# Kernel optimization log

Hardware: AMD Instinct MI355X
Metric: run time of the kernel (lower is better)

## Reference

```python
import jax, jax.numpy as jnp
from jax import lax
import numpy as np

KS = 15          # dark-channel window
PAD = (KS - 1) // 2
TEMP = 10000.0   # positional encoding temperature
NPF = 32         # max(num_pos_feats_x, y, z)
EPS = 1e-6


def _conv1x1(x, w, b):
    # x: [B,C,H,W], w: [O,C], b: [O]
    return jnp.einsum('bchw,oc->bohw', x, w) + b[None, :, None, None]


def _conv2s2(x, w, b):
    # kernel 2, stride 2, no padding; w: [O,I,2,2]
    y = lax.conv_general_dilated(x, w, (2, 2), 'VALID',
                                 dimension_numbers=('NCHW', 'OIHW', 'NCHW'))
    return y + b[None, :, None, None]


def _lrelu(x):
    return jnp.where(x >= 0, x, 0.1 * x)


def _resize(x, h, w):
    return jax.image.resize(x, (x.shape[0], x.shape[1], h, w), method='bilinear')


def _dark_channel(x):
    # min over channels, reflect pad, 15x15 sliding min (== unfold+min in torch)
    dm = jnp.min(x, axis=1, keepdims=True)  # [B,1,H,W]
    dm = jnp.pad(dm, ((0, 0), (0, 0), (PAD, PAD), (PAD, PAD)), mode='reflect')
    return lax.reduce_window(dm, jnp.inf, lax.min,
                             (1, 1, KS, KS), (1, 1, 1, 1), 'VALID')


def _sincos(e, d, dim_t):
    # e: [B,H,W] -> [B,H,W,d] with interleaved sin/cos (torch stack+flatten)
    p = e[..., None] / dim_t[:d]
    return jnp.stack((jnp.sin(p[..., 0::2]), jnp.cos(p[..., 1::2])),
                     axis=4).reshape(e.shape + (d,))


def _pos_encoding(x, dark):
    B, _, H, W = x.shape
    scale = 2.0 * np.pi
    yv = jnp.arange(H, dtype=jnp.float32)
    xv = jnp.arange(W, dtype=jnp.float32)
    ye = jnp.broadcast_to((yv / (yv[-1] + EPS) * scale)[None, :, None], (B, H, W))
    xe = jnp.broadcast_to((xv / (xv[-1] + EPS) * scale)[None, None, :], (B, H, W))
    z = dark[:, 0]
    ze = z / (jnp.max(z, axis=(1, 2), keepdims=True) + EPS) * scale
    dim_t = TEMP ** (2.0 * (jnp.arange(NPF, dtype=jnp.float32) // 2) / NPF)
    pos_x = _sincos(xe, 16, dim_t)
    pos_y = _sincos(ye, 16, dim_t)
    pos_z = _sincos(ze, 32, dim_t)
    return jnp.concatenate((pos_x, pos_y, pos_z), axis=3).transpose(0, 3, 1, 2)


def _forward(x, w_cf1, b_cf1, w_e1, b_e1, w_e2, b_e2, w_d1, b_d1, w_d2, b_d2,
             w_pha1, b_pha1, w_pha2, b_pha2, w_amp1, b_amp1, w_amp2, b_amp2,
             w_spat1, b_spat1, w_spat2, b_spat2, w_u1, b_u1, w_u2, b_u2,
             w_u3, b_u3, w_u4, b_u4, w_cf2, b_cf2, w_cf3, b_cf3):
    xori = x
    dark = _dark_channel(1.0 - x)            # DCP of inverted image [B,1,512,512]
    ape = _pos_encoding(x, dark) + _conv1x1(x, w_cf1, b_cf1)  # [B,64,H,W]

    x_f = _conv1x1(_conv1x1(x, w_e1, b_e1), w_e2, b_e2)       # [B,64,512,512]
    x_d1 = _conv2s2(x_f, w_d1, b_d1)                          # [B,128,256,256]
    x_d2 = _conv2s2(x_d1, w_d2, b_d2)                         # [B,256,128,128]
    Hd, Wd = x_d2.shape[2], x_d2.shape[3]

    x_freq = jnp.fft.rfft2(x_d2)             # norm='backward' (default)
    x_pha = jnp.angle(x_freq)
    x_amp = jnp.abs(x_freq)
    # phase branch is computed but unused downstream (matches original code)
    x_pha = _conv1x1(_lrelu(_conv1x1(x_pha, w_pha1, b_pha1)), w_pha2, b_pha2)
    x_amp = _conv1x1(_lrelu(_conv1x1(x_amp, w_amp1, b_amp1)), w_amp2, b_amp2)
    x_four = jnp.fft.irfft2(lax.complex(x_amp * jnp.cos(x_amp),
                                        x_amp * jnp.sin(x_amp)), s=(Hd, Wd))
    x_four = _conv1x1(_resize(x_four, x_d1.shape[2], x_d1.shape[3]), w_u1, b_u1)
    x_four = _conv1x1(_resize(x_four, x_f.shape[2], x_f.shape[3]), w_u2, b_u2)

    x_spat = _conv1x1(_lrelu(_conv1x1(x_d2, w_spat1, b_spat1)), w_spat2, b_spat2)
    x_spat = _conv1x1(_resize(x_spat, x_d1.shape[2], x_d1.shape[3]), w_u3, b_u3)
    x_spat = _conv1x1(_resize(x_spat, x_f.shape[2], x_f.shape[3]), w_u4, b_u4)
    x_spat = x_spat * ape

    four_spa = jnp.concatenate((x_four, x_spat), axis=1)      # [B,128,512,512]
    out = _conv1x1(_conv1x1(four_spa, w_cf2, b_cf2), w_cf3, b_cf3)
    return out + xori


def setup_inputs() -> dict:
    key = jax.random.key(0)
    ks = iter(jax.random.split(key, 64))
    def W(*shape):
        return 0.02 * jax.random.normal(next(ks), shape, dtype=jnp.float32)
    def Bb(n):
        return 0.01 * jax.random.normal(next(ks), (n,), dtype=jnp.float32)
    nc = 64
    inp = {'x': jax.random.uniform(next(ks), (1, 3, 512, 512), dtype=jnp.float32)}
    inp.update(w_cf1=W(nc, 3), b_cf1=Bb(nc))
    inp.update(w_e1=W(nc // 8, 3), b_e1=Bb(nc // 8))
    inp.update(w_e2=W(nc, nc // 8), b_e2=Bb(nc))
    inp.update(w_d1=W(2 * nc, nc, 2, 2), b_d1=Bb(2 * nc))
    inp.update(w_d2=W(4 * nc, 2 * nc, 2, 2), b_d2=Bb(4 * nc))
    for nm in ('pha', 'amp', 'spat'):
        inp['w_%s1' % nm] = W(4 * nc, 4 * nc); inp['b_%s1' % nm] = Bb(4 * nc)
        inp['w_%s2' % nm] = W(4 * nc, 4 * nc); inp['b_%s2' % nm] = Bb(4 * nc)
    inp.update(w_u1=W(2 * nc, 4 * nc), b_u1=Bb(2 * nc))
    inp.update(w_u2=W(nc, 2 * nc), b_u2=Bb(nc))
    inp.update(w_u3=W(2 * nc, 4 * nc), b_u3=Bb(2 * nc))
    inp.update(w_u4=W(nc, 2 * nc), b_u4=Bb(nc))
    inp.update(w_cf2=W(nc, 2 * nc), b_cf2=Bb(nc))
    inp.update(w_cf3=W(3, nc), b_cf3=Bb(3))
    return inp


def reference(x, w_cf1, b_cf1, w_e1, b_e1, w_e2, b_e2, w_d1, b_d1, w_d2, b_d2,
              w_pha1, b_pha1, w_pha2, b_pha2, w_amp1, b_amp1, w_amp2, b_amp2,
              w_spat1, b_spat1, w_spat2, b_spat2, w_u1, b_u1, w_u2, b_u2,
              w_u3, b_u3, w_u4, b_u4, w_cf2, b_cf2, w_cf3, b_cf3):
    return _forward(x, w_cf1, b_cf1, w_e1, b_e1, w_e2, b_e2, w_d1, b_d1,
                    w_d2, b_d2, w_pha1, b_pha1, w_pha2, b_pha2, w_amp1, b_amp1,
                    w_amp2, b_amp2, w_spat1, b_spat1, w_spat2, b_spat2,
                    w_u1, b_u1, w_u2, b_u2, w_u3, b_u3, w_u4, b_u4,
                    w_cf2, b_cf2, w_cf3, b_cf3)
```

## Files before the change

### kernel.cpp

```cpp
#include <hip/hip_runtime.h>
#include <math.h>

#define PI_F 3.14159265358979323846f
#define NPIX 262144

typedef __attribute__((ext_vector_type(8))) short sh8;
typedef __attribute__((ext_vector_type(4))) float fx4;
typedef __attribute__((ext_vector_type(4))) unsigned short ush4;

__device__ __forceinline__ unsigned short f2bf(float v) {
    unsigned u = __float_as_uint(v);
    return (unsigned short)((u + 0x7FFFu + ((u >> 16) & 1)) >> 16);
}
__device__ __forceinline__ float bf2f(unsigned short h) {
    return __uint_as_float((unsigned)h << 16);
}

__device__ __forceinline__ int refl512(int t) {
    if (t < 0) t = -t;
    if (t > 511) t = 1022 - t;
    return t;
}

__global__ __launch_bounds__(256) void k_mrow(const float* __restrict__ x, float* __restrict__ tmp,
                                              int* __restrict__ gmax) {
    __shared__ float row[512];
    int i = blockIdx.x, tid = threadIdx.x;
    if (i == 0 && tid == 0) gmax[0] = 0;
    #pragma unroll
    for (int h = 0; h < 2; h++) {
        int j = tid + h * 256;
        int p = (i << 9) + j;
        float m = fmaxf(x[p], fmaxf(x[p + NPIX], x[p + 2 * NPIX]));
        row[j] = 1.0f - m;
    }
    __syncthreads();
    #pragma unroll
    for (int h = 0; h < 2; h++) {
        int j = tid + h * 256;
        float m = 1e30f;
        #pragma unroll
        for (int d = -7; d <= 7; d++) m = fminf(m, row[refl512(j + d)]);
        tmp[(i << 9) + j] = m;
    }
}

__global__ __launch_bounds__(256) void k_mincol_max(const float* __restrict__ tmp, float* __restrict__ dark,
                                                    int* __restrict__ gmax) {
    int p = blockIdx.x * 256 + threadIdx.x;
    int i = p >> 9, j = p & 511;
    float m = 1e30f;
    #pragma unroll
    for (int d = -7; d <= 7; d++) m = fminf(m, tmp[(refl512(i + d) << 9) + j]);
    dark[p] = m;
    __shared__ float red[256];
    int tid = threadIdx.x;
    red[tid] = m;
    __syncthreads();
    for (int s = 128; s > 0; s >>= 1) {
        if (tid < s) red[tid] = fmaxf(red[tid], red[tid + s]);
        __syncthreads();
    }
    if (tid == 0) atomicMax(gmax, __float_as_int(red[0]));
}

__device__ __forceinline__ void prep_one(const float* __restrict__ w, unsigned short* __restrict__ h,
                                         unsigned short* __restrict__ l, int N, int K, int cshift, int idx) {
    if (idx >= N * K) return;
    int n = idx / K, kord = idx - n * K;
    int ksrc = kord;
    if (cshift) {
        int dydx = kord >> cshift, c = kord & ((1 << cshift) - 1);
        ksrc = c * 4 + dydx;
    }
    float v = w[n * K + ksrc];
    unsigned short hb = f2bf(v);
    h[idx] = hb;
    if (l) l[idx] = f2bf(v - bf2f(hb));
}

__global__ __launch_bounds__(256) void k_prepA(
    const float* __restrict__ w_d2, unsigned short* __restrict__ d2h, unsigned short* __restrict__ d2l,
    const float* __restrict__ w_a1, unsigned short* __restrict__ a1h, unsigned short* __restrict__ a1l,
    const float* __restrict__ w_a2, unsigned short* __restrict__ a2h, unsigned short* __restrict__ a2l,
    const float* __restrict__ w_s1, unsigned short* __restrict__ s1h,
    unsigned short* __restrict__ BfH, unsigned short* __restrict__ BfL,
    unsigned short* __restrict__ BfcH, unsigned short* __restrict__ BfcL,
    unsigned short* __restrict__ BicH, unsigned short* __restrict__ BicL,
    unsigned short* __restrict__ BirH, unsigned short* __restrict__ BirL,
    float* __restrict__ zbias) {
    int b = blockIdx.x, tid = threadIdx.x;
    if (b < 512)       { prep_one(w_d2, d2h, d2l, 256, 512, 7, b * 256 + tid); return; }
    else if (b < 768)  { prep_one(w_a1, a1h, a1l, 256, 256, 0, (b - 512) * 256 + tid); return; }
    else if (b < 1024) { prep_one(w_a2, a2h, a2l, 256, 256, 0, (b - 768) * 256 + tid); return; }
    else if (b < 1280) { prep_one(w_s1, s1h, nullptr, 256, 256, 0, (b - 1024) * 256 + tid); return; }
    int idx = (b - 1280) * 256 + tid;
    if (idx < 256) zbias[idx] = 0.f;
    const float w0 = 2.f * PI_F / 128.f;
    float v;
    unsigned short *H, *L;
    int off;
    if (idx < 32768) {
        int n = idx >> 7, k = idx & 127;
        int t = n & 127, r = (t * k) & 127;
        float s_, c_; sincosf(w0 * r, &s_, &c_);
        v = (n < 128) ? c_ : -s_;
        H = BfH; L = BfL; off = idx;
    } else if (idx < 98304) {
        int i = idx - 32768;
        int n = i >> 8, j = i & 255;
        int t = n & 127, r = (t * (j & 127)) & 127;
        float s_, c_; sincosf(w0 * r, &s_, &c_);
        v = (n < 128) ? ((j < 128) ? c_ : s_) : ((j < 128) ? -s_ : c_);
        H = BfcH; L = BfcL; off = i;
    } else if (idx < 163840) {
        int i = idx - 98304;
        int n = i >> 8, j = i & 255;
        int t = n & 127, r = (t * (j & 127)) & 127;
        float s_, c_; sincosf(w0 * r, &s_, &c_);
        v = ((n < 128) ? ((j < 128) ? c_ : -s_) : ((j < 128) ? s_ : c_)) * (1.f / 128.f);
        H = BicH; L = BicL; off = i;
    } else if (idx < 184320) {
        int i = idx - 163840;
        int col = i / 160, j = i - col * 160;
        if (j == 0) v = 1.f / 128.f;
        else if (j < 64)  { int r = (j * col) & 127; float s_, c_; sincosf(w0 * r, &s_, &c_); v = 2.f * c_ / 128.f; }
        else if (j == 64) v = (col & 1) ? -1.f / 128.f : 1.f / 128.f;
        else if (j >= 66 && j <= 128) { int k = j - 65; int r = (k * col) & 127; float s_, c_; sincosf(w0 * r, &s_, &c_); v = -2.f * s_ / 128.f; }
        else v = 0.f;
        H = BirH; L = BirL; off = i;
    } else return;
    unsigned short hb = f2bf(v);
    H[off] = hb;
    L[off] = f2bf(v - bf2f(hb));
}

__global__ __launch_bounds__(256) void k_prepB(
    const float* __restrict__ w_u3, const float* __restrict__ w_u4, float* __restrict__ Uf,
    const float* __restrict__ w_e1, const float* __restrict__ b_e1,
    const float* __restrict__ w_e2, const float* __restrict__ b_e2,
    const float* __restrict__ w_d1, const float* __restrict__ b_d1,
    unsigned short* __restrict__ d1ch, float* __restrict__ b1c,
    const float* __restrict__ b_u3, const float* __restrict__ b_u4, float* __restrict__ b43,
    const float* __restrict__ w2, const float* __restrict__ b2,
    const float* __restrict__ w3, const float* __restrict__ b3,
    const float* __restrict__ wu2, const float* __restrict__ bu2,
    const float* __restrict__ wu1, const float* __restrict__ bu1,
    float* __restrict__ Wc, float* __restrict__ bc,
    float* __restrict__ W21c, float* __restrict__ b21c) {
    int b = blockIdx.x, tid = threadIdx.x;
    if (b < 64) {
        int idx = b * 256 + tid;
        int n = idx >> 8, j = idx & 255;
        float s = 0.f;
        #pragma unroll 16
        for (int o = 0; o < 128; o++) s += w_u4[n * 128 + o] * w_u3[o * 256 + j];
        Uf[idx] = s;
    } else if (b < 80) {
        __shared__ float E[192];
        if (tid < 192) {
            int o = tid / 3, ci = tid - o * 3;
            float s = 0.f;
            #pragma unroll
            for (int r = 0; r < 8; r++) s += w_e2[o * 8 + r] * w_e1[r * 3 + ci];
            E[tid] = s;
        }
        __syncthreads();
        int idx = (b - 64) * 256 + tid;
        int n = idx >> 5, k = idx & 31;
        float s = 0.f;
        if (k < 12) {
            int dydx = k / 3, ci = k - dydx * 3;
            #pragma unroll 16
            for (int o = 0; o < 64; o++) s += w_d1[n * 256 + o * 4 + dydx] * E[o * 3 + ci];
        }
        d1ch[idx] = f2bf(s);
    } else if (b == 80) {
        __shared__ float f[64];
        if (tid < 64) {
            int o = tid;
            float s = b_e2[o];
            #pragma unroll
            for (int r = 0; r < 8; r++) s += w_e2[o * 8 + r] * b_e1[r];
            f[o] = s;
        }
        __syncthreads();
        if (tid < 128) {
            float s = b_d1[tid];
            #pragma unroll 8
            for (int o = 0; o < 64; o++) {
                float fo = f[o];
                #pragma unroll
                for (int dydx = 0; dydx < 4; dydx++) s += w_d1[tid * 256 + o * 4 + dydx] * fo;
            }
            b1c[tid] = s;
        }
    } else if (b == 81) {
        if (tid < 64) {
            float s = b_u4[tid];
            #pragma unroll 16
            for (int o = 0; o < 128; o++) s += w_u4[tid * 128 + o] * b_u3[o];
            b43[tid] = s;
        }
    } else {
        __shared__ float sWc[384], sW2c[384];
        if (tid < 128) {
            int j = tid;
            for (int r = 0; r < 3; r++) {
                float s = 0.f;
                #pragma unroll 16
                for (int o = 0; o < 64; o++) s += w3[r * 64 + o] * w2[o * 128 + j];
                sWc[r * 128 + j] = s;
                Wc[r * 128 + j] = s;
            }
            if (j < 3) {
                float s = b3[j];
                #pragma unroll 16
                for (int o = 0; o < 64; o++) s += w3[j * 64 + o] * b2[o];
                bc[j] = s;
            }
        }
        __syncthreads();
        if (tid < 128) {
            int j = tid;
            for (int r = 0; r < 3; r++) {
                float s = 0.f;
                #pragma unroll 16
                for (int o = 0; o < 64; o++) s += sWc[r * 128 + o] * wu2[o * 128 + j];
                sW2c[r * 128 + j] = s;
            }
        }
        __syncthreads();
        if (tid < 256) {
            int j = tid;
            for (int r = 0; r < 3; r++) {
                float s = 0.f;
                #pragma unroll 16
                for (int o = 0; o < 128; o++) s += sW2c[r * 128 + o] * wu1[o * 256 + j];
                W21c[r * 256 + j] = s;
            }
        }
        if (tid < 3) {
            float s = 0.f;
            #pragma unroll 16
            for (int o = 0; o < 128; o++) s += sW2c[tid * 128 + o] * bu1[o];
            #pragma unroll 16
            for (int o = 0; o < 64; o++)  s += sWc[tid * 128 + o] * bu2[o];
            b21c[tid] = s;
        }
    }
}

__global__ __launch_bounds__(256) void k_prep2(const float* __restrict__ Uf, const float* __restrict__ wsp2,
                                               const float* __restrict__ bsp2, const float* __restrict__ b43,
                                               unsigned short* __restrict__ Wg, float* __restrict__ bgc) {
    __shared__ float u[256], red[256];
    int n = blockIdx.x, tid = threadIdx.x;
    u[tid] = Uf[n * 256 + tid];
    __syncthreads();
    float s = 0.f;
    #pragma unroll 16
    for (int o = 0; o < 256; o++) s += u[o] * wsp2[o * 256 + tid];
    Wg[n * 256 + tid] = f2bf(s);
    red[tid] = u[tid] * bsp2[tid];
    __syncthreads();
    for (int st = 128; st > 0; st >>= 1) {
        if (tid < st) red[tid] += red[tid + st];
        __syncthreads();
    }
    if (tid == 0) bgc[n] = b43[n] + red[0];
}

template<int AMODE, int SPLIT, int LRELU, int TSTORE, int ABF16, int CBF16>
__global__ __launch_bounds__(256) void k_mmcf(const void* __restrict__ Asrc_,
                                              const unsigned short* __restrict__ Bh,
                                              const unsigned short* __restrict__ Bl,
                                              const float* __restrict__ bias, void* __restrict__ C_,
                                              int M, int N, int K, int cshift, int wshift, int srcW,
                                              int gy) {
    const float* Af = (const float*)Asrc_;
    const unsigned short* A16 = (const unsigned short*)Asrc_;
    float* Cf = (float*)C_;
    unsigned short* C16 = (unsigned short*)C_;
    __shared__ unsigned short AhS[128 * 40];
    __shared__ unsigned short BhS[64 * 40];
    __shared__ unsigned short AlS[SPLIT ? 128 * 40 : 8];
    __shared__ unsigned short BlS[SPLIT ? 64 * 40 : 8];
    int tid = threadIdx.x;
    int nwg = (int)gridDim.x;
    int bid = blockIdx.x;
    int qq = nwg >> 3, rr = nwg & 7;
    int xcd = bid & 7, ixw = bid >> 3;
    int work = (xcd < rr) ? (xcd * (qq + 1) + ixw) : (rr * (qq + 1) + (xcd - rr) * qq + ixw);
    int bx = work / gy;
    int by = work - bx * gy;
    int m0 = bx * 128;
    int n0 = by * 64;
    int wave = tid >> 6, lane = tid & 63;
    int wm = (wave >> 1) * 64, wn = (wave & 1) * 32;
    int l15 = lane & 15, quad = lane >> 4;
    int lk = quad * 8, lk4 = quad * 4;
    fx4 acc[4][2];
    #pragma unroll
    for (int a = 0; a < 4; a++)
        #pragma unroll
        for (int b = 0; b < 2; b++)
            acc[a][b] = (fx4){0.f, 0.f, 0.f, 0.f};

    int mm = tid & 127;
    int kpb = tid >> 7;
    int gm = m0 + mm;
    int oj = 0, oi = 0, cA = 0, kfA = 0, tauA = 0;
    size_t abase = 0;
    if (AMODE == 1) { oj = gm & ((1 << wshift) - 1); oi = gm >> wshift; }
    if (AMODE == 2) { oj = gm & 255; oi = gm >> 8; }
    if (AMODE == 3) abase = (size_t)gm * K;
    if (AMODE == 7) { cA = gm / 65; kfA = gm - cA * 65; }
    if (AMODE == 8) { cA = gm >> 7; tauA = gm & 127; }
    if (AMODE == 9) { cA = gm / 65; kfA = gm - cA * 65; }

    for (int kb = 0; kb < K; kb += 32) {
        if (AMODE == 3 && ABF16 && !SPLIT) {
            #pragma unroll
            for (int half = 0; half < 2; half++) {
                sh8 hv = *(const sh8*)(const void*)&A16[abase + kb + kpb * 16 + half * 8];
                *(sh8*)(void*)&AhS[mm * 40 + (kpb * 2 + half) * 8] = hv;
            }
        } else {
            #pragma unroll
            for (int half = 0; half < 2; half++) {
                sh8 hv, lv;
                #pragma unroll
                for (int tt = 0; tt < 4; tt++) {
                    int kp = kpb * 8 + half * 4 + tt;
                    int k0 = kb + kp * 2;
                    unsigned short h0, h1;
                    if (ABF16) {
                        size_t ad0, ad1;
                        if (AMODE == 0) {
                            ad0 = (size_t)k0 * M + gm;
                            ad1 = ad0 + M;
                        } else if (AMODE == 1) {
                            int c = k0 & ((1 << cshift) - 1);
                            int dydx = k0 >> cshift;
                            int dy = dydx >> 1, dx = dydx & 1;
                            size_t pix = (size_t)(2 * oi + dy) * srcW + (2 * oj + dx);
                            size_t plane = (size_t)srcW * srcW;
                            ad0 = (size_t)c * plane + pix;
                            ad1 = ad0 + plane;
                        } else if (AMODE == 3) {
                            ad0 = abase + k0;
                            ad1 = ad0 + 1;
                        } else if (AMODE == 7) {
                            int t0 = k0 & 127, hf = k0 >> 7;
                            ad0 = (size_t)(cA * 128 + t0) * 256 + hf * 128 + kfA;
                            ad1 = ad0 + 256;
                        } else {
                            int j0 = k0, j1 = k0 + 1;
                            int kf0 = (j0 < 65) ? j0 : ((j0 < 130) ? j0 - 65 : 0);
                            int hf0 = (j0 >= 65 && j0 < 130) ? 1 : 0;
                            int kf1 = (j1 < 65) ? j1 : ((j1 < 130) ? j1 - 65 : 0);
                            int hf1 = (j1 >= 65 && j1 < 130) ? 1 : 0;
                            ad0 = (size_t)(cA * 65 + kf0) * 256 + hf0 * 128 + tauA;
                            ad1 = (size_t)(cA * 65 + kf1) * 256 + hf1 * 128 + tauA;
                        }
                        h0 = A16[ad0];
                        h1 = A16[ad1];
                    } else {
                        float a0, a1;
                        if (AMODE == 2) {
                            if (k0 < 12) {
                                int d0 = k0 / 3, c0 = k0 - d0 * 3;
                                int k1 = k0 + 1;
                                int d1x = k1 / 3, c1 = k1 - d1x * 3;
                                a0 = Af[(size_t)c0 * NPIX + (size_t)(2 * oi + (d0 >> 1)) * 512 + 2 * oj + (d0 & 1)];
                                a1 = Af[(size_t)c1 * NPIX + (size_t)(2 * oi + (d1x >> 1)) * 512 + 2 * oj + (d1x & 1)];
                            } else { a0 = 0.f; a1 = 0.f; }
                        } else if (AMODE == 9) {
                            size_t ad = (size_t)cA * 16640 + (size_t)k0 * 65 + kfA;
                            float re0 = Af[ad], im0 = Af[ad + 2129920];
                            float re1 = Af[ad + 65], im1 = Af[ad + 65 + 2129920];
                            a0 = sqrtf(re0 * re0 + im0 * im0);
                            a1 = sqrtf(re1 * re1 + im1 * im1);
                        } else {
                            size_t ad0 = (size_t)k0 * M + gm;
                            a0 = Af[ad0];
                            a1 = Af[ad0 + M];
                        }
                        h0 = f2bf(a0);
                        h1 = f2bf(a1);
                        if (SPLIT) {
                            lv[tt * 2] = (short)f2bf(a0 - bf2f(h0));
                            lv[tt * 2 + 1] = (short)f2bf(a1 - bf2f(h1));
                        }
                    }
                    hv[tt * 2] = (short)h0;
                    hv[tt * 2 + 1] = (short)h1;
                }
                int coff = (kpb * 2 + half) * 8;
                *(sh8*)(void*)&AhS[mm * 40 + coff] = hv;
                if (SPLIT) *(sh8*)(void*)&AlS[mm * 40 + coff] = lv;
            }
        }
        {
            int n = tid >> 2, seg = tid & 3;
            size_t gb = (size_t)(n0 + n) * K + kb + seg * 8;
            *(sh8*)(void*)&BhS[n * 40 + seg * 8] = *(const sh8*)(const void*)&Bh[gb];
            if (SPLIT) *(sh8*)(void*)&BlS[n * 40 + seg * 8] = *(const sh8*)(const void*)&Bl[gb];
        }
        __syncthreads();
        sh8 af[4], bf[2], afl[4], bfl[2];
        #pragma unroll
        for (int mt = 0; mt < 4; mt++) {
            af[mt] = *(const sh8*)(const void*)&AhS[(wm + mt * 16 + l15) * 40 + lk];
            if (SPLIT) afl[mt] = *(const sh8*)(const void*)&AlS[(wm + mt * 16 + l15) * 40 + lk];
        }
        #pragma unroll
        for (int nt = 0; nt < 2; nt++) {
            bf[nt] = *(const sh8*)(const void*)&BhS[(wn + nt * 16 + l15) * 40 + lk];
            if (SPLIT) bfl[nt] = *(const sh8*)(const void*)&BlS[(wn + nt * 16 + l15) * 40 + lk];
        }
        #pragma unroll
        for (int mt = 0; mt < 4; mt++)
            #pragma unroll
            for (int nt = 0; nt < 2; nt++) {
                acc[mt][nt] = __builtin_amdgcn_mfma_f32_16x16x32_bf16(af[mt], bf[nt], acc[mt][nt], 0, 0, 0);
                if (SPLIT) {
                    acc[mt][nt] = __builtin_amdgcn_mfma_f32_16x16x32_bf16(af[mt], bfl[nt], acc[mt][nt], 0, 0, 0);
                    acc[mt][nt] = __builtin_amdgcn_mfma_f32_16x16x32_bf16(afl[mt], bf[nt], acc[mt][nt], 0, 0, 0);
                }
            }
        __syncthreads();
    }
    #pragma unroll
    for (int nt = 0; nt < 2; nt++) {
        int n = n0 + wn + nt * 16 + l15;
        float bs = bias[n];
        #pragma unroll
        for (int mt = 0; mt < 4; mt++) {
            int mbase = m0 + wm + mt * 16 + lk4;
            if (TSTORE) {
                #pragma unroll
                for (int r = 0; r < 4; r++) {
                    float q = acc[mt][nt][r] + bs;
                    if (LRELU) q = (q < 0.f) ? 0.1f * q : q;
                    if (CBF16) C16[(size_t)(mbase + r) * N + n] = f2bf(q);
                    else       Cf[(size_t)(mbase + r) * N + n] = q;
                }
            } else if (CBF16) {
                ush4 v;
                #pragma unroll
                for (int r = 0; r < 4; r++) {
                    float q = acc[mt][nt][r] + bs;
                    if (LRELU) q = (q < 0.f) ? 0.1f * q : q;
                    v[r] = f2bf(q);
                }
                *(ush4*)(void*)&C16[(size_t)n * M + mbase] = v;
            } else {
                float4 v;
                float* vp = (float*)&v;
                #pragma unroll
                for (int r = 0; r < 4; r++) {
                    float q = acc[mt][nt][r] + bs;
                    if (LRELU) q = (q < 0.f) ? 0.1f * q : q;
                    vp[r] = q;
                }
                *(float4*)&Cf[(size_t)n * M + mbase] = v;
            }
        }
    }
}

__global__ __launch_bounds__(256) void k_zbuild(const float* __restrict__ A2, unsigned short* __restrict__ Z) {
    int idx = blockIdx.x * 256 + threadIdx.x;
    int ct = idx / 65, kf = idx - ct * 65;
    int c = ct >> 7, t = ct & 127;
    float a = A2[idx];
    float s_, c_;
    sincosf(a, &s_, &c_);
    size_t m = (size_t)c * 65 + kf;
    Z[(size_t)t * 16640 + m] = f2bf(a * c_);
    Z[2129920 + (size_t)t * 16640 + m] = f2bf(a * s_);
}

__global__ __launch_bounds__(64) void k_h3s(const float* __restrict__ I2T, const float* __restrict__ W21c,
                                            const float* __restrict__ b21c, float* __restrict__ h3s) {
    __shared__ float wa[768], bs[3];
    int tid = threadIdx.x;
    for (int i = tid; i < 768; i += 64) wa[i] = W21c[i];
    if (tid < 3) bs[tid] = b21c[tid];
    __syncthreads();
    int q = blockIdx.x * 64 + tid;
    float a0 = bs[0], a1 = bs[1], a2 = bs[2];
    #pragma unroll 4
    for (int c = 0; c < 256; c++) {
        float v = I2T[(size_t)c * 16384 + q];
        a0 += wa[c] * v;
        a1 += wa[256 + c] * v;
        a2 += wa[512 + c] * v;
    }
    h3s[q] = a0; h3s[16384 + q] = a1; h3s[32768 + q] = a2;
}

__global__ __launch_bounds__(256) void k_final(const float* __restrict__ x,
                                               const float* __restrict__ dark, const int* __restrict__ gmax,
                                               const float* __restrict__ wcf1, const float* __restrict__ bcf1,
                                               const float* __restrict__ Wc, const float* __restrict__ bc,
                                               const float* __restrict__ g4s, const float* __restrict__ h3s,
                                               float* __restrict__ out) {
    __shared__ float idimt[32], w1[192], b1[64], wb[192], bcs[3], posy[16];
    __shared__ float gyr[64][68];
    __shared__ float hyr[3][68];
    int tid = threadIdx.x;
    int bid = blockIdx.x;
    int i = bid >> 1;
    int j0 = (bid & 1) << 8;
    int j = j0 + tid;
    int p = (i << 9) + j;

    const float scale = 2.f * PI_F;
    float inv511 = scale / (511.f + 1e-6f);
    float ye = (float)i * inv511;

    if (tid < 32) idimt[tid] = 1.f / powf(10000.f, (float)(2 * (tid >> 1)) / 32.f);
    if (tid < 192) w1[tid] = wcf1[tid];
    if (tid < 64) b1[tid] = bcf1[tid];
    if (tid < 192) { int r = tid / 64, c = tid - (tid / 64) * 64; wb[tid] = Wc[r * 128 + 64 + c]; }
    if (tid < 3) bcs[tid] = bc[tid];
    __syncthreads();
    if (tid >= 32 && tid < 48) {
        int c = tid - 32;
        float e = ye * idimt[c];
        posy[c] = ((c & 1) == 0) ? __sinf(e) : __cosf(e);
    }

    int ky = i >> 2, ry = i & 3;
    int ym = (ky > 0) ? ky - 1 : 0, yp = (ky < 127) ? ky + 1 : 127;
    float wy0 = (ry == 0) ? .375f : (ry == 1) ? .1875f : (ry == 2) ? .0625f : 0.f;
    float wy1 = (ry == 0 || ry == 3) ? .625f : .75f;
    float wy2 = (ry == 0) ? 0.f : (ry == 1) ? .0625f : (ry == 2) ? .1875f : .375f;
    int base = j0 >> 2;
    int r0 = ym * 128, r1 = ky * 128, r2 = yp * 128;
    for (int idx = tid; idx < 64 * 66; idx += 256) {
        int c = idx / 66, t = idx - c * 66;
        int col = base - 1 + t;
        col = (col < 0) ? 0 : (col > 127) ? 127 : col;
        const float* gp = g4s + (size_t)c * 16384;
        gyr[c][t] = wy0 * gp[r0 + col] + wy1 * gp[r1 + col] + wy2 * gp[r2 + col];
    }
    for (int idx = tid; idx < 3 * 66; idx += 256) {
        int c = idx / 66, t = idx - c * 66;
        int col = base - 1 + t;
        col = (col < 0) ? 0 : (col > 127) ? 127 : col;
        const float* hp = h3s + (size_t)c * 16384;
        hyr[c][t] = wy0 * hp[r0 + col] + wy1 * hp[r1 + col] + wy2 * hp[r2 + col];
    }
    __syncthreads();

    float xe = (float)j * inv511;
    float gm = __int_as_float(gmax[0]);
    float ze = dark[p] / (gm + 1e-6f) * scale;
    float x0 = x[p], x1 = x[p + NPIX], x2 = x[p + 2 * NPIX];

    int rx = j & 3;
    int tx = tid >> 2;
    float wx0 = (rx == 0) ? .375f : (rx == 1) ? .1875f : (rx == 2) ? .0625f : 0.f;
    float wx1 = (rx == 0 || rx == 3) ? .625f : .75f;
    float wx2 = (rx == 0) ? 0.f : (rx == 1) ? .0625f : (rx == 2) ? .1875f : .375f;

    float a0 = 0.f, a1 = 0.f, a2 = 0.f;
    #pragma unroll 1
    for (int c = 0; c < 64; c++) {
        float pos;
        if (c < 16)      { float e = xe * idimt[c];      pos = ((c & 1) == 0) ? __sinf(e) : __cosf(e); }
        else if (c < 32) { pos = posy[c - 16]; }
        else             { float e = ze * idimt[c - 32]; pos = ((c & 1) == 0) ? __sinf(e) : __cosf(e); }
        float ape = pos + w1[c * 3] * x0 + w1[c * 3 + 1] * x1 + w1[c * 3 + 2] * x2 + b1[c];
        float gv = wx0 * gyr[c][tx] + wx1 * gyr[c][tx + 1] + wx2 * gyr[c][tx + 2];
        float s = gv * ape;
        a0 += wb[c] * s; a1 += wb[64 + c] * s; a2 += wb[128 + c] * s;
    }
    float f0 = wx0 * hyr[0][tx] + wx1 * hyr[0][tx + 1] + wx2 * hyr[0][tx + 2];
    float f1 = wx0 * hyr[1][tx] + wx1 * hyr[1][tx + 1] + wx2 * hyr[1][tx + 2];
    float f2 = wx0 * hyr[2][tx] + wx1 * hyr[2][tx + 1] + wx2 * hyr[2][tx + 2];
    out[p]            = a0 + f0 + bcs[0] + x0;
    out[NPIX + p]     = a1 + f1 + bcs[1] + x1;
    out[2 * NPIX + p] = a2 + f2 + bcs[2] + x2;
}

extern "C" void kernel_launch(void* const* d_in, const int* in_sizes, int n_in,
                              void* d_out, int out_size, void* d_ws, size_t ws_size,
                              hipStream_t stream) {
    const float* x      = (const float*)d_in[0];
    const float* w_cf1  = (const float*)d_in[1];  const float* b_cf1 = (const float*)d_in[2];
    const float* w_e1   = (const float*)d_in[3];  const float* b_e1  = (const float*)d_in[4];
    const float* w_e2   = (const float*)d_in[5];  const float* b_e2  = (const float*)d_in[6];
    const float* w_d1   = (const float*)d_in[7];  const float* b_d1  = (const float*)d_in[8];
    const float* w_d2   = (const float*)d_in[9];  const float* b_d2  = (const float*)d_in[10];
    const float* w_amp1 = (const float*)d_in[15]; const float* b_amp1 = (const float*)d_in[16];
    const float* w_amp2 = (const float*)d_in[17]; const float* b_amp2 = (const float*)d_in[18];
    const float* w_sp1  = (const float*)d_in[19]; const float* b_sp1  = (const float*)d_in[20];
    const float* w_sp2  = (const float*)d_in[21]; const float* b_sp2  = (const float*)d_in[22];
    const float* w_u1   = (const float*)d_in[23]; const float* b_u1   = (const float*)d_in[24];
    const float* w_u2   = (const float*)d_in[25]; const float* b_u2   = (const float*)d_in[26];
    const float* w_u3   = (const float*)d_in[27]; const float* b_u3   = (const float*)d_in[28];
    const float* w_u4   = (const float*)d_in[29]; const float* b_u4   = (const float*)d_in[30];
    const float* w_cf2  = (const float*)d_in[31]; const float* b_cf2  = (const float*)d_in[32];
    const float* w_cf3  = (const float*)d_in[33]; const float* b_cf3  = (const float*)d_in[34];
    float* out = (float*)d_out;

    char* ws = (char*)d_ws;
    constexpr size_t MiB = 1ull << 20;
    float*  dark   = (float*)(ws + 0 * MiB);
    float*  tmp    = (float*)(ws + 1 * MiB);
    int*    gmax   = (int*)  (ws + 2 * MiB);
    float*  Wc     = (float*)(ws + 2 * MiB + 1024);
    float*  bc     = (float*)(ws + 2 * MiB + 2560);
    float*  W21c   = (float*)(ws + 2 * MiB + 4096);
    float*  b21c   = (float*)(ws + 2 * MiB + 7168);
    float*  b43    = (float*)(ws + 2 * MiB + 7424);
    unsigned short* d1ch = (unsigned short*)(ws + 3 * MiB);
    float*  b1c    = (float*)(ws + 3 * MiB + 16384);
    float*  Uf     = (float*)(ws + 3 * MiB + 32768);
    unsigned short* Wg = (unsigned short*)(ws + 3 * MiB + 131072);
    float*  bgc    = (float*)(ws + 3 * MiB + 196608);
    unsigned short* xd1 = (unsigned short*)(ws + 67 * MiB);
    unsigned short* xd2 = (unsigned short*)(ws + 99 * MiB);
    unsigned short* F1T = (unsigned short*)(ws + 115 * MiB);
    float*  F2C    = (float*)(ws + 147 * MiB);
    float*  A1     = (float*)(ws + 173 * MiB);
    float*  A2     = (float*)(ws + 182 * MiB);
    unsigned short* Zbuf = (unsigned short*)(ws + 115 * MiB);
    unsigned short* I1T  = (unsigned short*)(ws + 132 * MiB);
    float*  I2T    = (float*)(ws + 149 * MiB);
    float*  h3s    = (float*)(ws + 11 * MiB);
    unsigned short* s1 = (unsigned short*)(ws + 31 * MiB);
    float*  g4s    = (float*)(ws + 87 * MiB);
    unsigned short* wb16 = (unsigned short*)(ws + 192 * MiB);
    unsigned short* d2h = wb16 + 65536,   * d2l = wb16 + 196608;
    unsigned short* a1h = wb16 + 327680,  * a1l = wb16 + 393216;
    unsigned short* a2h = wb16 + 458752,  * a2l = wb16 + 524288;
    unsigned short* s1h = wb16 + 589824;
    unsigned short* BfH = wb16 + 786432,  * BfL = wb16 + 819200;
    unsigned short* BfcH = wb16 + 851968, * BfcL = wb16 + 917504;
    unsigned short* BicH = wb16 + 983040, * BicL = wb16 + 1048576;
    unsigned short* BirH = wb16 + 1114112,* BirL = wb16 + 1134592;
    float* zbias = (float*)(ws + 195 * MiB + 512 * 1024);

    k_mrow<<<512, 256, 0, stream>>>(x, tmp, gmax);
    k_mincol_max<<<1024, 256, 0, stream>>>(tmp, dark, gmax);
    k_prepA<<<2000, 256, 0, stream>>>(w_d2, d2h, d2l, w_amp1, a1h, a1l, w_amp2, a2h, a2l, w_sp1, s1h,
                                      BfH, BfL, BfcH, BfcL, BicH, BicL, BirH, BirL, zbias);
    k_prepB<<<83, 256, 0, stream>>>(w_u3, w_u4, Uf,
                                    w_e1, b_e1, w_e2, b_e2, w_d1, b_d1, d1ch, b1c,
                                    b_u3, b_u4, b43,
                                    w_cf2, b_cf2, w_cf3, b_cf3, w_u2, b_u2, w_u1, b_u1,
                                    Wc, bc, W21c, b21c);
    k_prep2<<<64, 256, 0, stream>>>(Uf, w_sp2, b_sp2, b43, Wg, bgc);

    k_mmcf<2, 0, 0, 0, 0, 1><<<1024, 256, 0, stream>>>(x, d1ch, nullptr, b1c, xd1, 65536, 128, 32, 0, 0, 0, 2);
    k_mmcf<1, 0, 0, 0, 1, 1><<<512, 256, 0, stream>>>(xd1, d2h, nullptr, b_d2, xd2, 16384, 256, 512, 7, 7, 256, 4);

    k_mmcf<3, 0, 0, 1, 1, 1><<<1024, 256, 0, stream>>>(xd2, BfH, nullptr, zbias, F1T, 32768, 256, 128, 0, 0, 0, 4);
    k_mmcf<7, 0, 0, 0, 1, 0><<<520, 256, 0, stream>>>(F1T, BfcH, nullptr, zbias, F2C, 16640, 256, 256, 0, 0, 0, 4);
    k_mmcf<9, 1, 1, 0, 0, 0><<<260, 256, 0, stream>>>(F2C, a1h, a1l, b_amp1, A1, 8320, 256, 256, 0, 0, 0, 4);
    k_mmcf<0, 1, 0, 0, 0, 0><<<260, 256, 0, stream>>>(A1, a2h, a2l, b_amp2, A2, 8320, 256, 256, 0, 0, 0, 4);
    k_zbuild<<<8320, 256, 0, stream>>>(A2, Zbuf);
    k_mmcf<0, 0, 0, 1, 1, 1><<<520, 256, 0, stream>>>(Zbuf, BicH, nullptr, zbias, I1T, 16640, 256, 256, 0, 0, 0, 4);
    k_mmcf<8, 0, 0, 1, 1, 0><<<512, 256, 0, stream>>>(I1T, BirH, nullptr, zbias, I2T, 32768, 128, 160, 0, 0, 0, 2);

    k_h3s<<<256, 64, 0, stream>>>(I2T, W21c, b21c, h3s);

    k_mmcf<0, 0, 1, 0, 1, 1><<<512, 256, 0, stream>>>(xd2, s1h, nullptr, b_sp1, s1, 16384, 256, 256, 0, 0, 0, 4);
    k_mmcf<0, 0, 0, 0, 1, 0><<<128, 256, 0, stream>>>(s1, Wg, nullptr, bgc, g4s, 16384, 64, 256, 0, 0, 0, 1);

    k_final<<<1024, 256, 0, stream>>>(x, dark, gmax, w_cf1, b_cf1, Wc, bc, g4s, h3s, out);
}
```

Before: 356.8 us.

## Fold 256-to-3 channel projection before inverse real DFT, merge prep and dark kernels

```diff
diff --git a/kernel.cpp b/kernel.cpp
--- a/kernel.cpp
+++ b/kernel.cpp
@@ -22,40 +22,38 @@
     return t;
 }
 
-__global__ __launch_bounds__(256) void k_mrow(const float* __restrict__ x, float* __restrict__ tmp,
+__global__ __launch_bounds__(256) void k_dark(const float* __restrict__ x, float* __restrict__ dark,
                                               int* __restrict__ gmax) {
-    __shared__ float row[512];
+    __shared__ float rm[15][512];
+    __shared__ float hm[15][512];
+    __shared__ float red[256];
     int i = blockIdx.x, tid = threadIdx.x;
-    if (i == 0 && tid == 0) gmax[0] = 0;
-    #pragma unroll
-    for (int h = 0; h < 2; h++) {
-        int j = tid + h * 256;
-        int p = (i << 9) + j;
-        float m = fmaxf(x[p], fmaxf(x[p + NPIX], x[p + 2 * NPIX]));
-        row[j] = 1.0f - m;
+    for (int idx = tid; idx < 15 * 512; idx += 256) {
+        int rr = idx >> 9, j = idx & 511;
+        int row = refl512(i - 7 + rr);
+        int p = (row << 9) + j;
+        rm[rr][j] = 1.0f - fmaxf(x[p], fmaxf(x[p + NPIX], x[p + 2 * NPIX]));
     }
     __syncthreads();
+    for (int idx = tid; idx < 15 * 512; idx += 256) {
+        int rr = idx >> 9, j = idx & 511;
+        float m = 1e30f;
+        #pragma unroll
+        for (int d = -7; d <= 7; d++) m = fminf(m, rm[rr][refl512(j + d)]);
+        hm[rr][j] = m;
+    }
+    __syncthreads();
+    float best = -1e30f;
     #pragma unroll
     for (int h = 0; h < 2; h++) {
         int j = tid + h * 256;
         float m = 1e30f;
         #pragma unroll
-        for (int d = -7; d <= 7; d++) m = fminf(m, row[refl512(j + d)]);
-        tmp[(i << 9) + j] = m;
-    }
-}
-
-__global__ __launch_bounds__(256) void k_mincol_max(const float* __restrict__ tmp, float* __restrict__ dark,
-                                                    int* __restrict__ gmax) {
-    int p = blockIdx.x * 256 + threadIdx.x;
-    int i = p >> 9, j = p & 511;
-    float m = 1e30f;
-    #pragma unroll
-    for (int d = -7; d <= 7; d++) m = fminf(m, tmp[(refl512(i + d) << 9) + j]);
-    dark[p] = m;
-    __shared__ float red[256];
-    int tid = threadIdx.x;
-    red[tid] = m;
+        for (int rr = 0; rr < 15; rr++) m = fminf(m, hm[rr][j]);
+        dark[(i << 9) + j] = m;
+        best = fmaxf(best, m);
+    }
+    red[tid] = best;
     __syncthreads();
     for (int s = 128; s > 0; s >>= 1) {
         if (tid < s) red[tid] = fmaxf(red[tid], red[tid + s]);
@@ -84,16 +82,27 @@
     const float* __restrict__ w_a1, unsigned short* __restrict__ a1h, unsigned short* __restrict__ a1l,
     const float* __restrict__ w_a2, unsigned short* __restrict__ a2h, unsigned short* __restrict__ a2l,
     const float* __restrict__ w_s1, unsigned short* __restrict__ s1h,
+    const float* __restrict__ w_u3, const float* __restrict__ w_u4, float* __restrict__ Uf,
     unsigned short* __restrict__ BfH, unsigned short* __restrict__ BfL,
     unsigned short* __restrict__ BfcH, unsigned short* __restrict__ BfcL,
     unsigned short* __restrict__ BicH, unsigned short* __restrict__ BicL,
-    unsigned short* __restrict__ BirH, unsigned short* __restrict__ BirL,
-    float* __restrict__ zbias) {
+    float* __restrict__ Birf,
+    float* __restrict__ zbias, int* __restrict__ gmax) {
     int b = blockIdx.x, tid = threadIdx.x;
+    if (b == 0 && tid == 0) gmax[0] = 0;
     if (b < 512)       { prep_one(w_d2, d2h, d2l, 256, 512, 7, b * 256 + tid); return; }
     else if (b < 768)  { prep_one(w_a1, a1h, a1l, 256, 256, 0, (b - 512) * 256 + tid); return; }
     else if (b < 1024) { prep_one(w_a2, a2h, a2l, 256, 256, 0, (b - 768) * 256 + tid); return; }
     else if (b < 1280) { prep_one(w_s1, s1h, nullptr, 256, 256, 0, (b - 1024) * 256 + tid); return; }
+    else if (b >= 2000) {
+        int idx = (b - 2000) * 256 + tid;
+        int n = idx >> 8, j = idx & 255;
+        float s = 0.f;
+        #pragma unroll 16
+        for (int o = 0; o < 128; o++) s += w_u4[n * 128 + o] * w_u3[o * 256 + j];
+        Uf[idx] = s;
+        return;
+    }
     int idx = (b - 1280) * 256 + tid;
     if (idx < 256) zbias[idx] = 0.f;
     const float w0 = 2.f * PI_F / 128.f;
@@ -121,14 +130,15 @@
         v = ((n < 128) ? ((j < 128) ? c_ : -s_) : ((j < 128) ? s_ : c_)) * (1.f / 128.f);
         H = BicH; L = BicL; off = i;
     } else if (idx < 184320) {
-        int i = idx - 163840;
-        int col = i / 160, j = i - col * 160;
+        int i2 = idx - 163840;
+        int col = i2 / 160, j = i2 - col * 160;
         if (j == 0) v = 1.f / 128.f;
         else if (j < 64)  { int r = (j * col) & 127; float s_, c_; sincosf(w0 * r, &s_, &c_); v = 2.f * c_ / 128.f; }
         else if (j == 64) v = (col & 1) ? -1.f / 128.f : 1.f / 128.f;
         else if (j >= 66 && j <= 128) { int k = j - 65; int r = (k * col) & 127; float s_, c_; sincosf(w0 * r, &s_, &c_); v = -2.f * s_ / 128.f; }
         else v = 0.f;
-        H = BirH; L = BirL; off = i;
+        Birf[j * 128 + col] = v;
+        return;
     } else return;
     unsigned short hb = f2bf(v);
     H[off] = hb;
@@ -136,12 +146,14 @@
 }
 
 __global__ __launch_bounds__(256) void k_prepB(
-    const float* __restrict__ w_u3, const float* __restrict__ w_u4, float* __restrict__ Uf,
+    const float* __restrict__ Uf,
     const float* __restrict__ w_e1, const float* __restrict__ b_e1,
     const float* __restrict__ w_e2, const float* __restrict__ b_e2,
     const float* __restrict__ w_d1, const float* __restrict__ b_d1,
     unsigned short* __restrict__ d1ch, float* __restrict__ b1c,
-    const float* __restrict__ b_u3, const float* __restrict__ b_u4, float* __restrict__ b43,
+    const float* __restrict__ w_u4, const float* __restrict__ b_u3, const float* __restrict__ b_u4,
+    const float* __restrict__ wsp2, const float* __restrict__ bsp2,
+    unsigned short* __restrict__ Wg, float* __restrict__ bgc,
     const float* __restrict__ w2, const float* __restrict__ b2,
     const float* __restrict__ w3, const float* __restrict__ b3,
     const float* __restrict__ wu2, const float* __restrict__ bu2,
@@ -149,14 +161,7 @@
     float* __restrict__ Wc, float* __restrict__ bc,
     float* __restrict__ W21c, float* __restrict__ b21c) {
     int b = blockIdx.x, tid = threadIdx.x;
-    if (b < 64) {
-        int idx = b * 256 + tid;
-        int n = idx >> 8, j = idx & 255;
-        float s = 0.f;
-        #pragma unroll 16
-        for (int o = 0; o < 128; o++) s += w_u4[n * 128 + o] * w_u3[o * 256 + j];
-        Uf[idx] = s;
-    } else if (b < 80) {
+    if (b < 16) {
         __shared__ float E[192];
         if (tid < 192) {
             int o = tid / 3, ci = tid - o * 3;
@@ -166,7 +171,7 @@
             E[tid] = s;
         }
         __syncthreads();
-        int idx = (b - 64) * 256 + tid;
+        int idx = b * 256 + tid;
         int n = idx >> 5, k = idx & 31;
         float s = 0.f;
         if (k < 12) {
@@ -175,7 +180,7 @@
             for (int o = 0; o < 64; o++) s += w_d1[n * 256 + o * 4 + dydx] * E[o * 3 + ci];
         }
         d1ch[idx] = f2bf(s);
-    } else if (b == 80) {
+    } else if (b == 16) {
         __shared__ float f[64];
         if (tid < 64) {
             int o = tid;
@@ -195,14 +200,7 @@
             }
             b1c[tid] = s;
         }
-    } else if (b == 81) {
-        if (tid < 64) {
-            float s = b_u4[tid];
-            #pragma unroll 16
-            for (int o = 0; o < 128; o++) s += w_u4[tid * 128 + o] * b_u3[o];
-            b43[tid] = s;
-        }
-    } else {
+    } else if (b == 17) {
         __shared__ float sWc[384], sW2c[384];
         if (tid < 128) {
             int j = tid;
@@ -248,27 +246,25 @@
             for (int o = 0; o < 64; o++)  s += sWc[tid * 128 + o] * bu2[o];
             b21c[tid] = s;
         }
-    }
-}
-
-__global__ __launch_bounds__(256) void k_prep2(const float* __restrict__ Uf, const float* __restrict__ wsp2,
-                                               const float* __restrict__ bsp2, const float* __restrict__ b43,
-                                               unsigned short* __restrict__ Wg, float* __restrict__ bgc) {
-    __shared__ float u[256], red[256];
-    int n = blockIdx.x, tid = threadIdx.x;
-    u[tid] = Uf[n * 256 + tid];
-    __syncthreads();
-    float s = 0.f;
-    #pragma unroll 16
-    for (int o = 0; o < 256; o++) s += u[o] * wsp2[o * 256 + tid];
-    Wg[n * 256 + tid] = f2bf(s);
-    red[tid] = u[tid] * bsp2[tid];
-    __syncthreads();
-    for (int st = 128; st > 0; st >>= 1) {
-        if (tid < st) red[tid] += red[tid + st];
-        __syncthreads();
-    }
-    if (tid == 0) bgc[n] = b43[n] + red[0];
+    } else {
+        int n = b - 18;
+        __shared__ float u[256], red[256];
+        u[tid] = Uf[n * 256 + tid];
+        __syncthreads();
+        float s = 0.f;
+        #pragma unroll 16
+        for (int o = 0; o < 256; o++) s += u[o] * wsp2[o * 256 + tid];
+        Wg[n * 256 + tid] = f2bf(s);
+        float rv = u[tid] * bsp2[tid];
+        if (tid < 128) rv += w_u4[n * 128 + tid] * b_u3[tid];
+        red[tid] = rv;
+        __syncthreads();
+        for (int st = 128; st > 0; st >>= 1) {
+            if (tid < st) red[tid] += red[tid + st];
+            __syncthreads();
+        }
+        if (tid == 0) bgc[n] = b_u4[n] + red[0];
+    }
 }
 
 template<int AMODE, int SPLIT, int LRELU, int TSTORE, int ABF16, int CBF16>
@@ -316,7 +312,6 @@
     if (AMODE == 2) { oj = gm & 255; oi = gm >> 8; }
     if (AMODE == 3) abase = (size_t)gm * K;
     if (AMODE == 7) { cA = gm / 65; kfA = gm - cA * 65; }
-    if (AMODE == 8) { cA = gm >> 7; tauA = gm & 127; }
     if (AMODE == 9) { cA = gm / 65; kfA = gm - cA * 65; }
 
     for (int kb = 0; kb < K; kb += 32) {
@@ -351,18 +346,10 @@
                         } else if (AMODE == 3) {
                             ad0 = abase + k0;
                             ad1 = ad0 + 1;
-                        } else if (AMODE == 7) {
+                        } else {
                             int t0 = k0 & 127, hf = k0 >> 7;
                             ad0 = (size_t)(cA * 128 + t0) * 256 + hf * 128 + kfA;
                             ad1 = ad0 + 256;
-                        } else {
-                            int j0 = k0, j1 = k0 + 1;
-                            int kf0 = (j0 < 65) ? j0 : ((j0 < 130) ? j0 - 65 : 0);
-                            int hf0 = (j0 >= 65 && j0 < 130) ? 1 : 0;
-                            int kf1 = (j1 < 65) ? j1 : ((j1 < 130) ? j1 - 65 : 0);
-                            int hf1 = (j1 >= 65 && j1 < 130) ? 1 : 0;
-                            ad0 = (size_t)(cA * 65 + kf0) * 256 + hf0 * 128 + tauA;
-                            ad1 = (size_t)(cA * 65 + kf1) * 256 + hf1 * 128 + tauA;
                         }
                         h0 = A16[ad0];
                         h1 = A16[ad1];
@@ -483,23 +470,50 @@
     Z[2129920 + (size_t)t * 16640 + m] = f2bf(a * s_);
 }
 
-__global__ __launch_bounds__(64) void k_h3s(const float* __restrict__ I2T, const float* __restrict__ W21c,
-                                            const float* __restrict__ b21c, float* __restrict__ h3s) {
-    __shared__ float wa[768], bs[3];
-    int tid = threadIdx.x;
-    for (int i = tid; i < 768; i += 64) wa[i] = W21c[i];
-    if (tid < 3) bs[tid] = b21c[tid];
+__global__ __launch_bounds__(256) void k_pfold(const unsigned short* __restrict__ I1T,
+                                               const float* __restrict__ W21c, float* __restrict__ P) {
+    __shared__ float wa[768];
+    int kf = blockIdx.x, tid = threadIdx.x;
+    for (int t = tid; t < 768; t += 256) wa[t] = W21c[t];
     __syncthreads();
-    int q = blockIdx.x * 64 + tid;
-    float a0 = bs[0], a1 = bs[1], a2 = bs[2];
+    float a0 = 0.f, a1 = 0.f, a2 = 0.f;
     #pragma unroll 4
     for (int c = 0; c < 256; c++) {
-        float v = I2T[(size_t)c * 16384 + q];
+        float v = bf2f(I1T[(size_t)(c * 65 + kf) * 256 + tid]);
         a0 += wa[c] * v;
         a1 += wa[256 + c] * v;
         a2 += wa[512 + c] * v;
     }
-    h3s[q] = a0; h3s[16384 + q] = a1; h3s[32768 + q] = a2;
+    P[(size_t)(0 * 65 + kf) * 256 + tid] = a0;
+    P[(size_t)(1 * 65 + kf) * 256 + tid] = a1;
+    P[(size_t)(2 * 65 + kf) * 256 + tid] = a2;
+}
+
+__global__ __launch_bounds__(128) void k_h3f(const float* __restrict__ P, const float* __restrict__ Birf,
+                                             const float* __restrict__ b21c, float* __restrict__ h3s) {
+    __shared__ float sp[390];
+    __shared__ float bs[3];
+    int tau = blockIdx.x, col = threadIdx.x;
+    for (int t = col; t < 390; t += 128) {
+        int r = t / 130, rem = t - r * 130;
+        int hf = rem / 65, kf = rem - hf * 65;
+        sp[t] = P[(size_t)(r * 65 + kf) * 256 + hf * 128 + tau];
+    }
+    if (col < 3) bs[col] = b21c[col];
+    __syncthreads();
+    float f0 = 0.f, f1 = 0.f, f2 = 0.f;
+    for (int k0 = 0; k0 < 130; k0++) {
+        float w = Birf[k0 * 128 + col];
+        int hf = (k0 >= 65) ? 1 : 0;
+        int base = hf ? (65 + k0 - 65) : k0;
+        f0 += w * sp[base];
+        f1 += w * sp[130 + base];
+        f2 += w * sp[260 + base];
+    }
+    size_t q = (size_t)tau * 128 + col;
+    h3s[q]         = f0 + bs[0];
+    h3s[16384 + q] = f1 + bs[1];
+    h3s[32768 + q] = f2 + bs[2];
 }
 
 __global__ __launch_bounds__(256) void k_final(const float* __restrict__ x,
@@ -612,13 +626,11 @@
     char* ws = (char*)d_ws;
     constexpr size_t MiB = 1ull << 20;
     float*  dark   = (float*)(ws + 0 * MiB);
-    float*  tmp    = (float*)(ws + 1 * MiB);
     int*    gmax   = (int*)  (ws + 2 * MiB);
     float*  Wc     = (float*)(ws + 2 * MiB + 1024);
     float*  bc     = (float*)(ws + 2 * MiB + 2560);
     float*  W21c   = (float*)(ws + 2 * MiB + 4096);
     float*  b21c   = (float*)(ws + 2 * MiB + 7168);
-    float*  b43    = (float*)(ws + 2 * MiB + 7424);
     unsigned short* d1ch = (unsigned short*)(ws + 3 * MiB);
     float*  b1c    = (float*)(ws + 3 * MiB + 16384);
     float*  Uf     = (float*)(ws + 3 * MiB + 32768);
@@ -632,7 +644,7 @@
     float*  A2     = (float*)(ws + 182 * MiB);
     unsigned short* Zbuf = (unsigned short*)(ws + 115 * MiB);
     unsigned short* I1T  = (unsigned short*)(ws + 132 * MiB);
-    float*  I2T    = (float*)(ws + 149 * MiB);
+    float*  P      = (float*)(ws + 149 * MiB);
     float*  h3s    = (float*)(ws + 11 * MiB);
     unsigned short* s1 = (unsigned short*)(ws + 31 * MiB);
     float*  g4s    = (float*)(ws + 87 * MiB);
@@ -644,19 +656,18 @@
     unsigned short* BfH = wb16 + 786432,  * BfL = wb16 + 819200;
     unsigned short* BfcH = wb16 + 851968, * BfcL = wb16 + 917504;
     unsigned short* BicH = wb16 + 983040, * BicL = wb16 + 1048576;
-    unsigned short* BirH = wb16 + 1114112,* BirL = wb16 + 1134592;
     float* zbias = (float*)(ws + 195 * MiB + 512 * 1024);
-
-    k_mrow<<<512, 256, 0, stream>>>(x, tmp, gmax);
-    k_mincol_max<<<1024, 256, 0, stream>>>(tmp, dark, gmax);
-    k_prepA<<<2000, 256, 0, stream>>>(w_d2, d2h, d2l, w_amp1, a1h, a1l, w_amp2, a2h, a2l, w_sp1, s1h,
-                                      BfH, BfL, BfcH, BfcL, BicH, BicL, BirH, BirL, zbias);
-    k_prepB<<<83, 256, 0, stream>>>(w_u3, w_u4, Uf,
+    float* Birf  = (float*)(ws + 196 * MiB);
+
+    k_prepA<<<2064, 256, 0, stream>>>(w_d2, d2h, d2l, w_amp1, a1h, a1l, w_amp2, a2h, a2l, w_sp1, s1h,
+                                      w_u3, w_u4, Uf,
+                                      BfH, BfL, BfcH, BfcL, BicH, BicL, Birf, zbias, gmax);
+    k_dark<<<512, 256, 0, stream>>>(x, dark, gmax);
+    k_prepB<<<82, 256, 0, stream>>>(Uf,
                                     w_e1, b_e1, w_e2, b_e2, w_d1, b_d1, d1ch, b1c,
-                                    b_u3, b_u4, b43,
+                                    w_u4, b_u3, b_u4, w_sp2, b_sp2, Wg, bgc,
                                     w_cf2, b_cf2, w_cf3, b_cf3, w_u2, b_u2, w_u1, b_u1,
                                     Wc, bc, W21c, b21c);
-    k_prep2<<<64, 256, 0, stream>>>(Uf, w_sp2, b_sp2, b43, Wg, bgc);
 
     k_mmcf<2, 0, 0, 0, 0, 1><<<1024, 256, 0, stream>>>(x, d1ch, nullptr, b1c, xd1, 65536, 128, 32, 0, 0, 0, 2);
     k_mmcf<1, 0, 0, 0, 1, 1><<<512, 256, 0, stream>>>(xd1, d2h, nullptr, b_d2, xd2, 16384, 256, 512, 7, 7, 256, 4);
@@ -667,9 +678,9 @@
     k_mmcf<0, 1, 0, 0, 0, 0><<<260, 256, 0, stream>>>(A1, a2h, a2l, b_amp2, A2, 8320, 256, 256, 0, 0, 0, 4);
     k_zbuild<<<8320, 256, 0, stream>>>(A2, Zbuf);
     k_mmcf<0, 0, 0, 1, 1, 1><<<520, 256, 0, stream>>>(Zbuf, BicH, nullptr, zbias, I1T, 16640, 256, 256, 0, 0, 0, 4);
-    k_mmcf<8, 0, 0, 1, 1, 0><<<512, 256, 0, stream>>>(I1T, BirH, nullptr, zbias, I2T, 32768, 128, 160, 0, 0, 0, 2);
-
-    k_h3s<<<256, 64, 0, stream>>>(I2T, W21c, b21c, h3s);
+
+    k_pfold<<<65, 256, 0, stream>>>(I1T, W21c, P);
+    k_h3f<<<128, 128, 0, stream>>>(P, Birf, b21c, h3s);
 
     k_mmcf<0, 0, 1, 0, 1, 1><<<512, 256, 0, stream>>>(xd2, s1h, nullptr, b_sp1, s1, 16384, 256, 256, 0, 0, 0, 4);
     k_mmcf<0, 0, 0, 0, 1, 0><<<128, 256, 0, stream>>>(s1, Wg, nullptr, bgc, g4s, 16384, 64, 256, 0, 0, 0, 1);
```

Measured after the change: 345.0 us. 3.3% less time.
